# Kernel optimization log

Hardware: AMD Instinct MI355X
Metric: run time of the kernel (lower is better)

Reference implementation:

```python
import jax, jax.numpy as jnp
import numpy as np

B, TQ, TK = 64, 1, 2048
QD, KD, U, H = 512, 512, 1024, 8
D = U // H  # per-head dim = 128


def setup_inputs() -> dict:
    key0 = jax.random.key(0)
    k0, k1, k2, k3, k4 = jax.random.split(key0, 5)
    query = jax.random.normal(k0, (B, TQ, QD), jnp.float32)
    key = jax.random.normal(k1, (B, TK, KD), jnp.float32)
    # 1x1 Conv1d == Linear: weight [out_ch, in_ch], bias [out_ch]
    Wq = jax.random.normal(k2, (U, QD), jnp.float32) / np.sqrt(QD).astype(np.float32)
    bq = jnp.zeros((U,), jnp.float32)
    Wk = jax.random.normal(k3, (U, KD), jnp.float32) / np.sqrt(KD).astype(np.float32)
    bk = jnp.zeros((U,), jnp.float32)
    # v is generated with torch.randn every forward in the original (unlearned);
    # here it is a fixed random vector of size D (per-head units).
    v = jax.random.normal(k4, (D,), jnp.float32)
    return {"query": query, "key": key, "Wq": Wq, "bq": bq, "Wk": Wk, "bk": bk, "v": v}


def reference(query, key, Wq, bq, Wk, bk, v):
    # 1x1 conv projections (channels-last linear)
    q = jnp.einsum('btq,uq->btu', query, Wq) + bq          # [B,TQ,U]
    k = jnp.einsum('btk,uk->btu', key, Wk) + bk            # [B,TK,U]
    # split heads: torch.stack(torch.split(x, D, dim=2), dim=1) -> [B,H,T,D]
    qs = q.reshape(B, TQ, H, D).transpose(0, 2, 1, 3)      # [B,H,TQ,D]
    ks = k.reshape(B, TK, H, D).transpose(0, 2, 1, 3)      # [B,H,TK,D]
    # weight-normalized random projection vector (b is zeros, folded away)
    g = np.float32(1.0) / np.sqrt(D).astype(np.float32)
    normed_v = g * v * jax.lax.rsqrt(jnp.sum(v * v))       # [D]
    # additive score: sum_d normed_v * tanh(ks + qs)  (qs broadcasts over TK)
    add = jnp.einsum('d,bhtd->bht', normed_v, jnp.tanh(ks + qs))  # [B,H,TK]
    # F.softmax without dim on a 4D tensor -> legacy dim=1 (heads axis)
    weights = jax.nn.softmax(add[:, :, None, :], axis=1)   # [B,H,TQ,TK]
    # value = unprojected key, shared across heads
    context = jnp.einsum('bhqt,btd->bhqd', weights, key)   # [B,H,TQ,KD]
    # view(B, TQ, -1): valid because TQ == 1
    return context.reshape(B, TQ, H * KD)
```

## Files before the change

### kernel.cpp

```cpp
#include <hip/hip_runtime.h>

#define B_   64
#define TK_  2048
#define KD_  512
#define U_   1024
#define H_   8
#define D_   128
#define MT   64
#define APAD 8
#define ASTR (KD_ + APAD)
#define NTILE (TK_ / MT)
#define GRID (B_ * NTILE)

typedef float f32x4 __attribute__((ext_vector_type(4)));
typedef short short8 __attribute__((ext_vector_type(8)));

__device__ __forceinline__ short f2bf(float f) {
    unsigned u = __float_as_uint(f);
    u += 0x7fffu + ((u >> 16) & 1u);
    return (short)(u >> 16);
}
__device__ __forceinline__ float bf2f(short s) {
    return __uint_as_float(((unsigned)(unsigned short)s) << 16);
}
__device__ __forceinline__ float tanh_fast(float x) {
    float e = __builtin_amdgcn_exp2f(x * 2.885390081777927f);
    return 1.0f - 2.0f * __builtin_amdgcn_rcpf(1.0f + e);
}

__global__ void nv_kernel(const float* __restrict__ v, float* __restrict__ wsNV) {
    __shared__ float red[D_];
    int tid = threadIdx.x;
    float x = v[tid];
    red[tid] = x * x;
    __syncthreads();
    if (tid == 0) {
        float s = 0.f;
        for (int i = 0; i < D_; ++i) s += red[i];
        red[0] = rsqrtf(s) * 0.08838834764831845f;
    }
    __syncthreads();
    wsNV[tid] = x * red[0];
}

__global__ void q_kernel(const float* __restrict__ query, const float* __restrict__ Wq,
                         const float* __restrict__ bq, const float* __restrict__ bk,
                         float* __restrict__ wsQ) {
    __shared__ float qrow[KD_];
    int b = blockIdx.x, ug = blockIdx.y, tid = threadIdx.x;
    if (tid < 128) ((float4*)qrow)[tid] = ((const float4*)(query + (size_t)b * KD_))[tid];
    __syncthreads();
    int u = ug * 256 + tid;
    const float4* wq = (const float4*)(Wq + (size_t)u * KD_);
    const float4* q4 = (const float4*)qrow;
    float acc = 0.f;
#pragma unroll 8
    for (int i = 0; i < KD_ / 4; ++i) {
        float4 a = q4[i], w = wq[i];
        acc += a.x * w.x + a.y * w.y + a.z * w.z + a.w * w.w;
    }
    wsQ[(size_t)b * U_ + u] = acc + bq[u] + bk[u];
}

__global__ void swz_kernel(const float* __restrict__ Wk, short* __restrict__ wsB) {
    int g = blockIdx.x * 256 + threadIdx.x;
    int slot = g >> 6, l = g & 63;
    int ublk = slot >> 4, ks = slot & 15;
    int u = ublk * 16 + (l & 15);
    int k0 = ks * 32 + ((l >> 4) << 3);
    const float* src = Wk + (size_t)u * KD_ + k0;
    short8 o;
#pragma unroll
    for (int j = 0; j < 8; ++j) o[j] = f2bf(src[j]);
    *(short8*)(wsB + (size_t)g * 8) = o;
}

template <bool ATOMIC>
__global__ __launch_bounds__(256, 2) void attn_kernel(
    const float* __restrict__ key, const short* __restrict__ wsB,
    const float* __restrict__ wsQ, const float* __restrict__ wsNV,
    float* __restrict__ outp)
{
    __shared__ short As[MT * ASTR];
    __shared__ float S[MT][H_];
    __shared__ float Wt[MT][H_];

    int bx = blockIdx.x;
    int b = bx & 63, tt = bx >> 6;
    int tid = threadIdx.x;

    const float4* src = (const float4*)(key + ((size_t)b * TK_ + (size_t)tt * MT) * KD_);
#pragma unroll 8
    for (int j = 0; j < 32; ++j) {
        int i = tid + j * 256;
        float4 v = src[i];
        int t = i >> 7, c4 = (i & 127) << 2;
        short4 h4;
        h4.x = f2bf(v.x); h4.y = f2bf(v.y); h4.z = f2bf(v.z); h4.w = f2bf(v.w);
        *(short4*)&As[t * ASTR + c4] = h4;
    }
    __syncthreads();

    int w = tid >> 6, l = tid & 63;
    int l15 = l & 15, lq = l >> 4;
    const short8* bp = (const short8*)wsB;

    for (int c = 0; c < 2; ++c) {
        int ub = c * 512 + w * 128;
        int ub16 = ub >> 4;
        int bidx = ub16 * 1024 + l;

        f32x4 acc[4][8] = {};

        short8 bc[8];
#pragma unroll
        for (int nf = 0; nf < 8; ++nf) bc[nf] = bp[bidx + nf * 1024];

#pragma unroll 1
        for (int ks = 0; ks < 16; ++ks) {
            short8 bn[8];
            if (ks < 15) {
#pragma unroll
                for (int nf = 0; nf < 8; ++nf) bn[nf] = bp[bidx + nf * 1024 + (ks + 1) * 64];
            }
            short8 a[4];
#pragma unroll
            for (int mf = 0; mf < 4; ++mf)
                a[mf] = *(const short8*)&As[(mf * 16 + l15) * ASTR + ks * 32 + (lq << 3)];
#pragma unroll
            for (int mf = 0; mf < 4; ++mf)
#pragma unroll
                for (int nf = 0; nf < 8; ++nf)
                    acc[mf][nf] = __builtin_amdgcn_mfma_f32_16x16x32_bf16(a[mf], bc[nf], acc[mf][nf], 0, 0, 0);
            if (ks < 15) {
#pragma unroll
                for (int nf = 0; nf < 8; ++nf) bc[nf] = bn[nf];
            }
        }

        float qv[8], nv[8];
#pragma unroll
        for (int nf = 0; nf < 8; ++nf) {
            int d = nf * 16 + l15;
            qv[nf] = wsQ[(size_t)b * U_ + ub + d];
            nv[nf] = wsNV[d];
        }
        int h = ub >> 7;
#pragma unroll
        for (int mf = 0; mf < 4; ++mf)
#pragma unroll
            for (int r = 0; r < 4; ++r) {
                float p = 0.f;
#pragma unroll
                for (int nf = 0; nf < 8; ++nf)
                    p += nv[nf] * tanh_fast(acc[mf][nf][r] + qv[nf]);
                p += __shfl_xor(p, 1);
                p += __shfl_xor(p, 2);
                p += __shfl_xor(p, 4);
                p += __shfl_xor(p, 8);
                if (l15 == 0) S[mf * 16 + lq * 4 + r][h] = p;
            }
    }
    __syncthreads();

    if (tid < MT) {
        float sv[H_];
        float mx = -1e30f;
#pragma unroll
        for (int h = 0; h < H_; ++h) { sv[h] = S[tid][h]; mx = fmaxf(mx, sv[h]); }
        float sum = 0.f;
#pragma unroll
        for (int h = 0; h < H_; ++h) {
            sv[h] = __builtin_amdgcn_exp2f((sv[h] - mx) * 1.4426950408889634f);
            sum += sv[h];
        }
        float inv = __builtin_amdgcn_rcpf(sum);
#pragma unroll
        for (int h = 0; h < H_; ++h) Wt[tid][h] = sv[h] * inv;
    }
    __syncthreads();

    int dg = (tid & 127) << 2;
    int hb = (tid >> 7) << 2;
    float cacc[4][4] = {};
    for (int t = 0; t < MT; ++t) {
        short4 kk = *(const short4*)&As[t * ASTR + dg];
        float k0 = bf2f(kk.x), k1 = bf2f(kk.y), k2 = bf2f(kk.z), k3 = bf2f(kk.w);
#pragma unroll
        for (int j = 0; j < 4; ++j) {
            float wt = Wt[t][hb + j];
            cacc[j][0] += wt * k0; cacc[j][1] += wt * k1;
            cacc[j][2] += wt * k2; cacc[j][3] += wt * k3;
        }
    }
    if (ATOMIC) {
        float* ob = outp + (size_t)b * (H_ * KD_);
#pragma unroll
        for (int j = 0; j < 4; ++j)
#pragma unroll
            for (int d = 0; d < 4; ++d)
                atomicAdd(&ob[(hb + j) * KD_ + dg + d], cacc[j][d]);
    } else {
        float* pb = outp + (size_t)bx * (H_ * KD_);
#pragma unroll
        for (int j = 0; j < 4; ++j)
            *(f32x4*)&pb[(hb + j) * KD_ + dg] = *(f32x4*)&cacc[j][0];
    }
}

__global__ void reduce_kernel(const float* __restrict__ partial, float* __restrict__ out) {
    int o = blockIdx.x * 256 + threadIdx.x;
    int b = o >> 10;
    int u4 = o & 1023;
    const f32x4* p4 = (const f32x4*)partial;
    f32x4 s = {0.f, 0.f, 0.f, 0.f};
#pragma unroll 8
    for (int tt = 0; tt < NTILE; ++tt)
        s += p4[((size_t)(tt * 64 + b)) * 1024 + u4];
    ((f32x4*)out)[o] = s;
}

extern "C" void kernel_launch(void* const* d_in, const int* in_sizes, int n_in,
                              void* d_out, int out_size, void* d_ws, size_t ws_size,
                              hipStream_t stream) {
    const float* query = (const float*)d_in[0];
    const float* key   = (const float*)d_in[1];
    const float* Wq    = (const float*)d_in[2];
    const float* bq    = (const float*)d_in[3];
    const float* Wk    = (const float*)d_in[4];
    const float* bk    = (const float*)d_in[5];
    const float* v     = (const float*)d_in[6];
    float* out = (float*)d_out;

    char* ws = (char*)d_ws;
    float* wsNV = (float*)ws;
    float* wsQ  = (float*)(ws + 4096);
    short* wsB  = (short*)(ws + 524288);
    float* wsP  = (float*)(ws + 2 * 1024 * 1024);

    size_t need = 2 * 1024 * 1024 + (size_t)GRID * (H_ * KD_) * sizeof(float);

    nv_kernel<<<1, 128, 0, stream>>>(v, wsNV);
    q_kernel<<<dim3(64, 4), 256, 0, stream>>>(query, Wq, bq, bk, wsQ);
    swz_kernel<<<256, 256, 0, stream>>>(Wk, wsB);

    if (ws_size >= need) {
        attn_kernel<false><<<GRID, 256, 0, stream>>>(key, wsB, wsQ, wsNV, wsP);
        reduce_kernel<<<256, 256, 0, stream>>>(wsP, out);
    } else {
        hipMemsetAsync(d_out, 0, (size_t)out_size * sizeof(float), stream);
        attn_kernel<true><<<GRID, 256, 0, stream>>>(key, wsB, wsQ, wsNV, out);
    }
}
```

Baseline: 528.9 us.

## Swizzle LDS key tile, split staging to overlap with GEMM, halve accumulators

Stores the bf16 key tile in LDS in an MFMA-fragment-ordered, XOR-swizzled layout without padding, so A-fragment reads are contiguous and free of bank conflicts. The tile is loaded in two halves: the second half is converted and written after the first eight k-steps of the GEMM, overlapping global loads with MFMA work. Each wave now processes 64 output columns per pass instead of 128, cutting the accumulator registers from 32 to 16 fragments, and the weighted-sum stage is reworked to 8-wide reads with two heads per thread. Barriers use a custom wait plus s_barrier, and holding 32 float4s in registers risks higher register pressure.

Measured after the change: 557.7 us. 1.05x slower.

```diff
diff --git a/kernel.cpp b/kernel.cpp
--- a/kernel.cpp
+++ b/kernel.cpp
@@ -7,8 +7,6 @@
 #define H_   8
 #define D_   128
 #define MT   64
-#define APAD 8
-#define ASTR (KD_ + APAD)
 #define NTILE (TK_ / MT)
 #define GRID (B_ * NTILE)
 
@@ -26,6 +24,23 @@
 __device__ __forceinline__ float tanh_fast(float x) {
     float e = __builtin_amdgcn_exp2f(x * 2.885390081777927f);
     return 1.0f - 2.0f * __builtin_amdgcn_rcpf(1.0f + e);
+}
+
+__device__ __forceinline__ void wg_barrier_lds() {
+    asm volatile("" ::: "memory");
+    __builtin_amdgcn_s_waitcnt(0xC07F);
+    __builtin_amdgcn_s_barrier();
+    asm volatile("" ::: "memory");
+}
+
+__device__ __forceinline__ void write_frag(short* As, int t, int c4, float4 v) {
+    int ks = c4 >> 5;
+    int lq = (c4 >> 3) & 3;
+    int E  = ((lq << 4) | (t & 15)) ^ (ks & 7);
+    int si = ((ks * 4 + (t >> 4)) << 9) + (E << 3) + (c4 & 4);
+    short4 h4;
+    h4.x = f2bf(v.x); h4.y = f2bf(v.y); h4.z = f2bf(v.z); h4.w = f2bf(v.w);
+    *(short4*)&As[si] = h4;
 }
 
 __global__ void nv_kernel(const float* __restrict__ v, float* __restrict__ wsNV) {
@@ -81,87 +96,134 @@
     const float* __restrict__ wsQ, const float* __restrict__ wsNV,
     float* __restrict__ outp)
 {
-    __shared__ short As[MT * ASTR];
+    __shared__ short As[MT * KD_];
     __shared__ float S[MT][H_];
     __shared__ float Wt[MT][H_];
 
     int bx = blockIdx.x;
     int b = bx & 63, tt = bx >> 6;
     int tid = threadIdx.x;
-
-    const float4* src = (const float4*)(key + ((size_t)b * TK_ + (size_t)tt * MT) * KD_);
-#pragma unroll 8
-    for (int j = 0; j < 32; ++j) {
-        int i = tid + j * 256;
-        float4 v = src[i];
-        int t = i >> 7, c4 = (i & 127) << 2;
-        short4 h4;
-        h4.x = f2bf(v.x); h4.y = f2bf(v.y); h4.z = f2bf(v.z); h4.w = f2bf(v.w);
-        *(short4*)&As[t * ASTR + c4] = h4;
-    }
-    __syncthreads();
-
     int w = tid >> 6, l = tid & 63;
-    int l15 = l & 15, lq = l >> 4;
+    int l15 = l & 15;
+
+    const float4* kt = (const float4*)(key + ((size_t)b * TK_ + (size_t)tt * MT) * KD_);
+
+    float4 h0v[16], h1v[16];
+#pragma unroll
+    for (int j = 0; j < 16; ++j) {
+        int idx = tid + j * 256;
+        h0v[j] = kt[((idx >> 6) << 7) + (idx & 63)];
+    }
+#pragma unroll
+    for (int j = 0; j < 16; ++j) {
+        int idx = tid + j * 256;
+        h1v[j] = kt[((idx >> 6) << 7) + (idx & 63) + 64];
+    }
+#pragma unroll
+    for (int j = 0; j < 16; ++j) {
+        int idx = tid + j * 256;
+        write_frag(As, idx >> 6, (idx & 63) << 2, h0v[j]);
+    }
+    wg_barrier_lds();
+
     const short8* bp = (const short8*)wsB;
 
-    for (int c = 0; c < 2; ++c) {
-        int ub = c * 512 + w * 128;
-        int ub16 = ub >> 4;
-        int bidx = ub16 * 1024 + l;
-
-        f32x4 acc[4][8] = {};
-
-        short8 bc[8];
-#pragma unroll
-        for (int nf = 0; nf < 8; ++nf) bc[nf] = bp[bidx + nf * 1024];
-
+    float ps[4][4];
+    f32x4 acc[4][4];
+    short8 bc[4], bn[4];
+    int bbase_cur = 0;
+
+    for (int p = 0; p < 4; ++p) {
+        int c = p >> 1, nh = p & 1;
+        int ub = c * 512 + w * 128 + nh * 64;
+        int bbase = (ub >> 4) * 1024 + l;
+        bbase_cur = bbase;
+
+        if (nh == 0) {
+#pragma unroll
+            for (int mf = 0; mf < 4; ++mf)
+#pragma unroll
+                for (int r = 0; r < 4; ++r) ps[mf][r] = 0.f;
+        }
+#pragma unroll
+        for (int mf = 0; mf < 4; ++mf)
+#pragma unroll
+            for (int nf = 0; nf < 4; ++nf) acc[mf][nf] = (f32x4){0.f, 0.f, 0.f, 0.f};
+
+#pragma unroll
+        for (int nf = 0; nf < 4; ++nf) bc[nf] = bp[bbase + nf * 1024];
+
+        auto gemm_seg = [&](int ks0, int ks1) {
 #pragma unroll 1
-        for (int ks = 0; ks < 16; ++ks) {
-            short8 bn[8];
-            if (ks < 15) {
-#pragma unroll
-                for (int nf = 0; nf < 8; ++nf) bn[nf] = bp[bidx + nf * 1024 + (ks + 1) * 64];
+            for (int ks = ks0; ks < ks1; ++ks) {
+                if (ks < 15) {
+#pragma unroll
+                    for (int nf = 0; nf < 4; ++nf)
+                        bn[nf] = bp[bbase_cur + nf * 1024 + (ks + 1) * 64];
+                }
+                int ab = ((ks * 4) << 9) + ((l ^ (ks & 7)) << 3);
+                short8 a[4];
+#pragma unroll
+                for (int mf = 0; mf < 4; ++mf)
+                    a[mf] = *(const short8*)&As[ab + (mf << 9)];
+#pragma unroll
+                for (int mf = 0; mf < 4; ++mf)
+#pragma unroll
+                    for (int nf = 0; nf < 4; ++nf)
+                        acc[mf][nf] = __builtin_amdgcn_mfma_f32_16x16x32_bf16(
+                            a[mf], bc[nf], acc[mf][nf], 0, 0, 0);
+                if (ks < 15) {
+#pragma unroll
+                    for (int nf = 0; nf < 4; ++nf) bc[nf] = bn[nf];
+                }
             }
-            short8 a[4];
+        };
+
+        if (p == 0) {
+            gemm_seg(0, 8);
+#pragma unroll
+            for (int j = 0; j < 16; ++j) {
+                int idx = tid + j * 256;
+                write_frag(As, idx >> 6, ((idx & 63) << 2) + 256, h1v[j]);
+            }
+            wg_barrier_lds();
+            gemm_seg(8, 16);
+        } else {
+            gemm_seg(0, 16);
+        }
+
+        float qv[4], nv[4];
+#pragma unroll
+        for (int nf = 0; nf < 4; ++nf) {
+            qv[nf] = wsQ[(size_t)b * U_ + ub + nf * 16 + l15];
+            nv[nf] = wsNV[nh * 64 + nf * 16 + l15];
+        }
+#pragma unroll
+        for (int mf = 0; mf < 4; ++mf)
+#pragma unroll
+            for (int r = 0; r < 4; ++r) {
+                float pp = ps[mf][r];
+#pragma unroll
+                for (int nf = 0; nf < 4; ++nf)
+                    pp += nv[nf] * tanh_fast(acc[mf][nf][r] + qv[nf]);
+                ps[mf][r] = pp;
+            }
+        if (nh == 1) {
+            int h = c * 4 + w;
 #pragma unroll
             for (int mf = 0; mf < 4; ++mf)
-                a[mf] = *(const short8*)&As[(mf * 16 + l15) * ASTR + ks * 32 + (lq << 3)];
-#pragma unroll
-            for (int mf = 0; mf < 4; ++mf)
-#pragma unroll
-                for (int nf = 0; nf < 8; ++nf)
-                    acc[mf][nf] = __builtin_amdgcn_mfma_f32_16x16x32_bf16(a[mf], bc[nf], acc[mf][nf], 0, 0, 0);
-            if (ks < 15) {
-#pragma unroll
-                for (int nf = 0; nf < 8; ++nf) bc[nf] = bn[nf];
-            }
-        }
-
-        float qv[8], nv[8];
-#pragma unroll
-        for (int nf = 0; nf < 8; ++nf) {
-            int d = nf * 16 + l15;
-            qv[nf] = wsQ[(size_t)b * U_ + ub + d];
-            nv[nf] = wsNV[d];
-        }
-        int h = ub >> 7;
-#pragma unroll
-        for (int mf = 0; mf < 4; ++mf)
-#pragma unroll
-            for (int r = 0; r < 4; ++r) {
-                float p = 0.f;
-#pragma unroll
-                for (int nf = 0; nf < 8; ++nf)
-                    p += nv[nf] * tanh_fast(acc[mf][nf][r] + qv[nf]);
-                p += __shfl_xor(p, 1);
-                p += __shfl_xor(p, 2);
-                p += __shfl_xor(p, 4);
-                p += __shfl_xor(p, 8);
-                if (l15 == 0) S[mf * 16 + lq * 4 + r][h] = p;
-            }
-    }
-    __syncthreads();
+#pragma unroll
+                for (int r = 0; r < 4; ++r) {
+                    float pp = ps[mf][r];
+                    pp += __shfl_xor(pp, 1);
+                    pp += __shfl_xor(pp, 2);
+                    pp += __shfl_xor(pp, 4);
+                    pp += __shfl_xor(pp, 8);
+                    if (l15 == 0) S[mf * 16 + (l >> 4) * 4 + r][h] = pp;
+                }
+        }
+    }
+    wg_barrier_lds();
 
     if (tid < MT) {
         float sv[H_];
@@ -178,33 +240,38 @@
 #pragma unroll
         for (int h = 0; h < H_; ++h) Wt[tid][h] = sv[h] * inv;
     }
-    __syncthreads();
-
-    int dg = (tid & 127) << 2;
-    int hb = (tid >> 7) << 2;
-    float cacc[4][4] = {};
+    wg_barrier_lds();
+
+    int dg8 = (tid & 63) << 3;
+    int hp = tid >> 6;
+    int vks = dg8 >> 5, vlq = (dg8 >> 3) & 3;
+    float cacc[2][8] = {};
+#pragma unroll 1
     for (int t = 0; t < MT; ++t) {
-        short4 kk = *(const short4*)&As[t * ASTR + dg];
-        float k0 = bf2f(kk.x), k1 = bf2f(kk.y), k2 = bf2f(kk.z), k3 = bf2f(kk.w);
-#pragma unroll
-        for (int j = 0; j < 4; ++j) {
-            float wt = Wt[t][hb + j];
-            cacc[j][0] += wt * k0; cacc[j][1] += wt * k1;
-            cacc[j][2] += wt * k2; cacc[j][3] += wt * k3;
+        int E = ((vlq << 4) | (t & 15)) ^ (vks & 7);
+        short8 kk = *(const short8*)&As[((vks * 4 + (t >> 4)) << 9) + (E << 3)];
+        float w0 = Wt[t][2 * hp], w1 = Wt[t][2 * hp + 1];
+#pragma unroll
+        for (int d = 0; d < 8; ++d) {
+            float kv = bf2f(kk[d]);
+            cacc[0][d] += w0 * kv;
+            cacc[1][d] += w1 * kv;
         }
     }
     if (ATOMIC) {
         float* ob = outp + (size_t)b * (H_ * KD_);
 #pragma unroll
-        for (int j = 0; j < 4; ++j)
-#pragma unroll
-            for (int d = 0; d < 4; ++d)
-                atomicAdd(&ob[(hb + j) * KD_ + dg + d], cacc[j][d]);
+        for (int j = 0; j < 2; ++j)
+#pragma unroll
+            for (int d = 0; d < 8; ++d)
+                atomicAdd(&ob[(2 * hp + j) * KD_ + dg8 + d], cacc[j][d]);
     } else {
         float* pb = outp + (size_t)bx * (H_ * KD_);
 #pragma unroll
-        for (int j = 0; j < 4; ++j)
-            *(f32x4*)&pb[(hb + j) * KD_ + dg] = *(f32x4*)&cacc[j][0];
+        for (int j = 0; j < 2; ++j) {
+            *(f32x4*)&pb[(2 * hp + j) * KD_ + dg8]     = *(f32x4*)&cacc[j][0];
+            *(f32x4*)&pb[(2 * hp + j) * KD_ + dg8 + 4] = *(f32x4*)&cacc[j][4];
+        }
     }
 }
 
```
